# Kernel optimization log

Hardware: AMD Instinct MI355X
Metric: run time of the kernel (lower is better)

Reference implementation:

```python
import jax, jax.numpy as jnp
import numpy as np


def setup_inputs() -> dict:
    key = jax.random.key(0)
    x = jax.random.normal(key, (8, 128, 64, 64), dtype=jnp.float32)
    return {"x": x}


def reference(x) -> jnp.ndarray:
    # x: [B, d, c, c]; original uses a raw view (row-major reshape), not a permute.
    B, d, c, _ = x.shape
    n = c * c
    fch = x.reshape(B, n, d)                      # [B, N, d] reinterpretation of memory
    # self-similarity attention (no scaling): softmax(fch @ fch^T)
    attn = jax.nn.softmax(jnp.einsum('bnd,bmd->bnm', fch, fch), axis=-1)  # [B, N, N]
    out = jnp.einsum('bnd,bnm->bdm', fch, attn)   # fch^T @ attn -> [B, d, N]
    return out.reshape(B, d, c, c)
```

## Files before the change

### kernel.cpp

```cpp
#include <hip/hip_runtime.h>


typedef __attribute__((ext_vector_type(8))) __bf16 bf16x8;
typedef __attribute__((ext_vector_type(4))) float f32x4;
typedef __attribute__((ext_vector_type(4))) unsigned int u32x4;

#define MFMA16(a, b, c) __builtin_amdgcn_mfma_f32_16x16x32_bf16((a), (b), (c), 0, 0, 0)
#define GLOAD16(g, l)                                                       \
  __builtin_amdgcn_global_load_lds(                                         \
      (const __attribute__((address_space(1))) void*)(g),                   \
      (__attribute__((address_space(3))) void*)(l), 16, 0, 0)
#define GLOAD4(g, l)                                                        \
  __builtin_amdgcn_global_load_lds(                                         \
      (const __attribute__((address_space(1))) void*)(g),                   \
      (__attribute__((address_space(3))) void*)(l), 4, 0, 0)

static constexpr int NT = 4096;
static constexpr int DD = 128;
static constexpr float L2E = 1.4426950408889634f;

__device__ __forceinline__ unsigned short bfc(float f) {
  return __builtin_bit_cast(unsigned short, (__bf16)f);
}
__device__ __forceinline__ float bf2f(unsigned short u) {
  return (float)__builtin_bit_cast(__bf16, u);
}

__global__ __launch_bounds__(256) void cab_prep(const float* __restrict__ x,
                                                ushort* __restrict__ Fbb,
                                                ushort* __restrict__ FtF,
                                                float* __restrict__ nrm,
                                                float* __restrict__ bmax) {
  const int blk = blockIdx.x;
  const int b = blk & 7, n0 = (blk >> 3) * 64;
  const float* F = x + ((size_t)b * NT + n0) * DD;
  ushort* Fo = Fbb + ((size_t)b * NT + n0) * DD;
  ushort* To = FtF + (size_t)b * DD * NT;

  __shared__ ushort T[128 * 68];
  __shared__ float redw[4];

  const int t = threadIdx.x, seg = t & 15, rl = t >> 4;
  float lmax = 0.f;

#pragma unroll
  for (int i = 0; i < 4; ++i) {
    const int r = i * 16 + rl;
    float4 u = *(const float4*)(F + (size_t)r * DD + seg * 8);
    float4 v = *(const float4*)(F + (size_t)r * DD + seg * 8 + 4);
    ushort w[8] = {bfc(u.x), bfc(u.y), bfc(u.z), bfc(u.w),
                   bfc(v.x), bfc(v.y), bfc(v.z), bfc(v.w)};
    *(ushort4*)(Fo + (size_t)r * DD + seg * 8) = make_ushort4(w[0], w[1], w[2], w[3]);
    *(ushort4*)(Fo + (size_t)r * DD + seg * 8 + 4) = make_ushort4(w[4], w[5], w[6], w[7]);
    float s = 0.f;
#pragma unroll
    for (int j = 0; j < 8; ++j) {
      T[(seg * 8 + j) * 68 + r] = w[j];
      float f = bf2f(w[j]);
      s = fmaf(f, f, s);
    }
#pragma unroll
    for (int off = 1; off < 16; off <<= 1) s += __shfl_xor(s, off, 64);
    float rn = sqrtf(s);
    if (seg == 0) nrm[(size_t)b * NT + n0 + r] = rn;
    lmax = fmaxf(lmax, rn);
  }
#pragma unroll
  for (int off = 1; off < 64; off <<= 1) lmax = fmaxf(lmax, __shfl_xor(lmax, off, 64));
  if ((t & 63) == 0) redw[t >> 6] = lmax;
  __syncthreads();
  if (t == 0) bmax[blk] = fmaxf(fmaxf(redw[0], redw[1]), fmaxf(redw[2], redw[3]));

#pragma unroll
  for (int i = 0; i < 4; ++i) {
    int idx = i * 256 + t;
    int nh = idx >> 9, dt = (idx >> 6) & 7, ln = idx & 63;
    int d = dt * 16 + (ln & 15), nl = nh * 32 + (ln >> 4) * 8;
    const ushort* p = &T[d * 68 + nl];
    uint2 q0 = *(const uint2*)p;
    uint2 q1 = *(const uint2*)(p + 4);
    u32x4 q = {q0.x, q0.y, q1.x, q1.y};
    *(u32x4*)(To + (size_t)(((n0 >> 6) * 2 + nh) * 8 + dt) * 512 + ln * 8) = q;
  }
}

__global__ __launch_bounds__(64) void cab_mx(const float* __restrict__ bmax,
                                             float* __restrict__ mxf) {
  const int b = blockIdx.x, l = threadIdx.x;
  float m = bmax[l * 8 + b];
#pragma unroll
  for (int off = 1; off < 64; off <<= 1) m = fmaxf(m, __shfl_xor(m, off, 64));
  if (l == 0) mxf[b] = m;
}

__global__ __launch_bounds__(256, 4) void cab_rowstats(const ushort* __restrict__ Fbb,
                                                       const float* __restrict__ nrm,
                                                       const float* __restrict__ mxf,
                                                       float* __restrict__ c2g) {
  const int b = blockIdx.x & 7;
  const int nb = (blockIdx.x >> 3) * 64;
  const ushort* Fb = Fbb + (size_t)b * NT * DD;

  const int t = threadIdx.x, lane = t & 63, wv = t >> 6;
  const int lcol = lane & 15, hi = lane >> 4;
  const int nh = wv >> 1, mq = wv & 1;

  __shared__ __align__(16) char FmB[2][16384];
  __shared__ float zred[64];

  int fmoff[4];
#pragma unroll
  for (int i = 0; i < 4; ++i) {
    int L = i * 256 + t;
    int m = L >> 4, c = (L & 15) ^ (m & 15);
    fmoff[i] = m * DD + c * 8;
  }

  bf16x8 afr[2][4];
#pragma unroll
  for (int nt = 0; nt < 2; ++nt)
#pragma unroll
    for (int ks = 0; ks < 4; ++ks)
      afr[nt][ks] = *(const bf16x8*)(Fb + (size_t)(nb + nh * 32 + nt * 16 + lcol) * DD +
                                     ks * 32 + hi * 8);

  const float mxv = mxf[b] * L2E;
  float nsh[8];
#pragma unroll
  for (int nt = 0; nt < 2; ++nt)
#pragma unroll
    for (int r = 0; r < 4; ++r)
      nsh[nt * 4 + r] = -nrm[(size_t)b * NT + nb + nh * 32 + nt * 16 + hi * 4 + r] * mxv;

#pragma unroll
  for (int i = 0; i < 4; ++i) GLOAD16(Fb + fmoff[i], &FmB[0][i * 4096 + wv * 1024]);
  __syncthreads();

  float zloc[8];
#pragma unroll
  for (int i = 0; i < 8; ++i) zloc[i] = 0.f;

  for (int s = 0; s < 64; ++s) {
    const int cur = s & 1;
    if (s < 63) {
      const ushort* src = Fb + (size_t)(s + 1) * 64 * DD;
#pragma unroll
      for (int i = 0; i < 4; ++i)
        GLOAD16(src + fmoff[i], &FmB[cur ^ 1][i * 4096 + wv * 1024]);
    }

    f32x4 sacc[2][2];
#pragma unroll
    for (int nt = 0; nt < 2; ++nt)
#pragma unroll
      for (int ms = 0; ms < 2; ++ms) sacc[nt][ms] = (f32x4){0.f, 0.f, 0.f, 0.f};
#pragma unroll
    for (int ms = 0; ms < 2; ++ms)
#pragma unroll
      for (int ks = 0; ks < 4; ++ks) {
        int ml = mq * 32 + ms * 16 + lcol;
        bf16x8 bb = *(const bf16x8*)&FmB[cur][ml * 256 + (((ks * 4 + hi) ^ lcol) << 4)];
#pragma unroll
        for (int nt = 0; nt < 2; ++nt) sacc[nt][ms] = MFMA16(afr[nt][ks], bb, sacc[nt][ms]);
      }
#pragma unroll
    for (int nt = 0; nt < 2; ++nt)
#pragma unroll
      for (int r = 0; r < 4; ++r)
        zloc[nt * 4 + r] += __builtin_amdgcn_exp2f(fmaf(sacc[nt][0][r], L2E, nsh[nt * 4 + r])) +
                            __builtin_amdgcn_exp2f(fmaf(sacc[nt][1][r], L2E, nsh[nt * 4 + r]));
    __syncthreads();
  }

#pragma unroll
  for (int i = 0; i < 8; ++i) {
#pragma unroll
    for (int off = 1; off < 16; off <<= 1) zloc[i] += __shfl_xor(zloc[i], off, 64);
  }
  if (mq == 1 && lcol == 0) {
#pragma unroll
    for (int i = 0; i < 8; ++i) zred[nh * 32 + (i >> 2) * 16 + hi * 4 + (i & 3)] = zloc[i];
  }
  __syncthreads();
  if (mq == 0 && lcol == 0) {
#pragma unroll
    for (int i = 0; i < 8; ++i) {
      int nloc = nh * 32 + (i >> 2) * 16 + hi * 4 + (i & 3);
      c2g[(size_t)b * NT + nb + nloc] = nsh[i] - __log2f(zloc[i] + zred[nloc]);
    }
  }
}

__global__ __launch_bounds__(256, 2) void cab_out(const ushort* __restrict__ Fbb,
                                                  const ushort* __restrict__ FtF,
                                                  const float* __restrict__ c2g,
                                                  float* __restrict__ out) {
  const int b = blockIdx.x & 7, mb0 = (blockIdx.x >> 3) * 64;
  const ushort* Fb = Fbb + (size_t)b * NT * DD;
  const ushort* Fr = FtF + (size_t)b * DD * NT;
  const float* c2p = c2g + (size_t)b * NT;

  const int t = threadIdx.x, lane = t & 63, wv = t >> 6;
  const int lcol = lane & 15, hi = lane >> 4;
  const int mh = wv & 1, nh = wv >> 1;

  __shared__ __align__(16) char LB[42496];
  char* FnB = LB;
  char* Wt = LB + 32768;
  float* c2l = (float*)(LB + 41984);

  int fnoff[4];
#pragma unroll
  for (int i = 0; i < 4; ++i) {
    int L = i * 256 + t;
    int n = L >> 4, cn = (L & 15) ^ (n & 15);
    fnoff[i] = n * DD + cn * 8;
  }

  bf16x8 fmf[2][4];
#pragma unroll
  for (int ms = 0; ms < 2; ++ms)
#pragma unroll
    for (int ks = 0; ks < 4; ++ks)
      fmf[ms][ks] = *(const bf16x8*)(Fb + (size_t)(mb0 + mh * 32 + ms * 16 + lcol) * DD +
                                     ks * 32 + hi * 8);

  f32x4 accO[8][2];
#pragma unroll
  for (int dt = 0; dt < 8; ++dt)
#pragma unroll
    for (int ms = 0; ms < 2; ++ms) accO[dt][ms] = (f32x4){0.f, 0.f, 0.f, 0.f};

#pragma unroll
  for (int i = 0; i < 4; ++i) GLOAD16(Fb + fnoff[i], &FnB[i * 4096 + wv * 1024]);
  if (wv == 0) GLOAD4(c2p + lane, &c2l[0]);
  __syncthreads();

  const unsigned wtbase = wv * 2304;
  const ushort* a2w = Fr + (size_t)(nh * 8) * 512 + lane * 8;

  for (int s = 0; s < 64; ++s) {
    const int cur = s & 1;

    const ushort* ap = a2w + (size_t)s * 8192;
    bf16x8 a2[8];
#pragma unroll
    for (int dt = 0; dt < 8; ++dt) a2[dt] = *(const bf16x8*)(ap + dt * 512);

    if (s < 63) {
      const ushort* fs = Fb + (size_t)(s + 1) * 64 * DD;
#pragma unroll
      for (int i = 0; i < 4; ++i)
        GLOAD16(fs + fnoff[i], &FnB[(cur ^ 1) * 16384 + i * 4096 + wv * 1024]);
      if (wv == 0) GLOAD4(c2p + (s + 1) * 64 + lane, &c2l[((s + 1) & 1) * 64]);
    }

    f32x4 sacc[2][2];
#pragma unroll
    for (int nt = 0; nt < 2; ++nt)
#pragma unroll
      for (int ms = 0; ms < 2; ++ms) sacc[nt][ms] = (f32x4){0.f, 0.f, 0.f, 0.f};
#pragma unroll
    for (int nt = 0; nt < 2; ++nt)
#pragma unroll
      for (int ks = 0; ks < 4; ++ks) {
        int n = (nh * 2 + nt) * 16 + lcol;
        bf16x8 a = *(const bf16x8*)&FnB[cur * 16384 + n * 256 +
                                        (((ks * 4 + hi) ^ lcol) << 4)];
#pragma unroll
        for (int ms = 0; ms < 2; ++ms) sacc[nt][ms] = MFMA16(a, fmf[ms][ks], sacc[nt][ms]);
      }

#pragma unroll
    for (int nt = 0; nt < 2; ++nt) {
      float4 cv = *(const float4*)&c2l[(s & 1) * 64 + nh * 32 + nt * 16 + hi * 4];
#pragma unroll
      for (int ms = 0; ms < 2; ++ms) {
        ushort4 wp;
        wp.x = bfc(__builtin_amdgcn_exp2f(fmaf(sacc[nt][ms][0], L2E, cv.x)));
        wp.y = bfc(__builtin_amdgcn_exp2f(fmaf(sacc[nt][ms][1], L2E, cv.y)));
        wp.z = bfc(__builtin_amdgcn_exp2f(fmaf(sacc[nt][ms][2], L2E, cv.z)));
        wp.w = bfc(__builtin_amdgcn_exp2f(fmaf(sacc[nt][ms][3], L2E, cv.w)));
        *(ushort4*)&Wt[wtbase + (ms * 16 + lcol) * 72 + nt * 32 + hi * 8] = wp;
      }
    }

    bf16x8 b2[2];
#pragma unroll
    for (int ms = 0; ms < 2; ++ms) {
      const char* p = &Wt[wtbase + (ms * 16 + lcol) * 72 + hi * 16];
      uint2 lo = *(const uint2*)p;
      uint2 h2 = *(const uint2*)(p + 8);
      b2[ms] = __builtin_bit_cast(bf16x8, (u32x4){lo.x, lo.y, h2.x, h2.y});
    }
#pragma unroll
    for (int dt = 0; dt < 8; ++dt)
#pragma unroll
      for (int ms = 0; ms < 2; ++ms) accO[dt][ms] = MFMA16(a2[dt], b2[ms], accO[dt][ms]);

    __syncthreads();
  }

  float* red = (float*)LB;
  if (nh == 1) {
#pragma unroll
    for (int dt = 0; dt < 8; ++dt)
#pragma unroll
      for (int ms = 0; ms < 2; ++ms)
#pragma unroll
        for (int r = 0; r < 4; ++r)
          red[mh * 4096 + (dt * 8 + ms * 4 + r) * 64 + lane] = accO[dt][ms][r];
  }
  __syncthreads();
  if (nh == 0) {
    float* Ob = out + (size_t)b * DD * NT;
#pragma unroll
    for (int dt = 0; dt < 8; ++dt)
#pragma unroll
      for (int ms = 0; ms < 2; ++ms)
#pragma unroll
        for (int r = 0; r < 4; ++r) {
          float v = accO[dt][ms][r] + red[mh * 4096 + (dt * 8 + ms * 4 + r) * 64 + lane];
          Ob[(size_t)(dt * 16 + hi * 4 + r) * NT + mb0 + mh * 32 + ms * 16 + lcol] = v;
        }
  }
}

extern "C" void kernel_launch(void* const* d_in, const int* in_sizes, int n_in,
                              void* d_out, int out_size, void* d_ws, size_t ws_size,
                              hipStream_t stream) {
  const float* x = (const float*)d_in[0];
  float* out = (float*)d_out;
  char* ws = (char*)d_ws;
  ushort* Fbb = (ushort*)ws;
  ushort* FtF = (ushort*)(ws + (8u << 20));
  float* nrm = (float*)(ws + (16u << 20));
  float* bmax = (float*)(ws + (16u << 20) + 131072);
  float* mxf = (float*)(ws + (16u << 20) + 133120);
  float* c2 = (float*)(ws + (16u << 20) + 134144);

  hipLaunchKernelGGL(cab_prep, dim3(512), dim3(256), 0, stream, x, Fbb, FtF, nrm, bmax);
  hipLaunchKernelGGL(cab_mx, dim3(8), dim3(64), 0, stream, bmax, mxf);
  hipLaunchKernelGGL(cab_rowstats, dim3(512), dim3(256), 0, stream, Fbb, nrm, mxf, c2);
  hipLaunchKernelGGL(cab_out, dim3(512), dim3(256), 0, stream, Fbb, FtF, c2, out);
}
```

Measured before the change: 132.0 us.

## Load score-GEMM operand rows directly from global into registers, drop LDS staging

The cab_out kernel previously staged each 64-row block of F and the c2 log-normaliser values into double-buffered LDS with async global_load_lds, followed by a block-wide barrier per iteration. Each wave now loads its own bf16x8 fragments of F and the c2 float4 values straight from global memory into registers, and the per-iteration __syncthreads is removed. LDS use shrinks to the per-wave W tile, which may allow more resident blocks. The cost is more global/L2 traffic, since the two mh waves now each fetch the same rows, plus exposed load latency without explicit prefetch. The Wt region is per-wave, so dropping the barrier looks safe.

```diff
diff --git a/kernel.cpp b/kernel.cpp
--- a/kernel.cpp
+++ b/kernel.cpp
@@ -10,10 +10,6 @@
   __builtin_amdgcn_global_load_lds(                                         \
       (const __attribute__((address_space(1))) void*)(g),                   \
       (__attribute__((address_space(3))) void*)(l), 16, 0, 0)
-#define GLOAD4(g, l)                                                        \
-  __builtin_amdgcn_global_load_lds(                                         \
-      (const __attribute__((address_space(1))) void*)(g),                   \
-      (__attribute__((address_space(3))) void*)(l), 4, 0, 0)
 
 static constexpr int NT = 4096;
 static constexpr int DD = 128;
@@ -204,18 +200,8 @@
   const int lcol = lane & 15, hi = lane >> 4;
   const int mh = wv & 1, nh = wv >> 1;
 
-  __shared__ __align__(16) char LB[42496];
-  char* FnB = LB;
-  char* Wt = LB + 32768;
-  float* c2l = (float*)(LB + 41984);
-
-  int fnoff[4];
-#pragma unroll
-  for (int i = 0; i < 4; ++i) {
-    int L = i * 256 + t;
-    int n = L >> 4, cn = (L & 15) ^ (n & 15);
-    fnoff[i] = n * DD + cn * 8;
-  }
+  __shared__ __align__(16) char LB[32768];
+  char* Wt = LB;
 
   bf16x8 fmf[2][4];
 #pragma unroll
@@ -231,29 +217,28 @@
 #pragma unroll
     for (int ms = 0; ms < 2; ++ms) accO[dt][ms] = (f32x4){0.f, 0.f, 0.f, 0.f};
 
-#pragma unroll
-  for (int i = 0; i < 4; ++i) GLOAD16(Fb + fnoff[i], &FnB[i * 4096 + wv * 1024]);
-  if (wv == 0) GLOAD4(c2p + lane, &c2l[0]);
-  __syncthreads();
-
   const unsigned wtbase = wv * 2304;
   const ushort* a2w = Fr + (size_t)(nh * 8) * 512 + lane * 8;
+  const ushort* a1w = Fb + (size_t)(nh * 32 + lcol) * DD + hi * 8;
+  const float* cw = c2p + nh * 32 + hi * 4;
 
   for (int s = 0; s < 64; ++s) {
-    const int cur = s & 1;
-
     const ushort* ap = a2w + (size_t)s * 8192;
     bf16x8 a2[8];
 #pragma unroll
     for (int dt = 0; dt < 8; ++dt) a2[dt] = *(const bf16x8*)(ap + dt * 512);
 
-    if (s < 63) {
-      const ushort* fs = Fb + (size_t)(s + 1) * 64 * DD;
-#pragma unroll
-      for (int i = 0; i < 4; ++i)
-        GLOAD16(fs + fnoff[i], &FnB[(cur ^ 1) * 16384 + i * 4096 + wv * 1024]);
-      if (wv == 0) GLOAD4(c2p + (s + 1) * 64 + lane, &c2l[((s + 1) & 1) * 64]);
-    }
+    const ushort* rp = a1w + (size_t)s * 64 * DD;
+    bf16x8 a1[2][4];
+#pragma unroll
+    for (int nt = 0; nt < 2; ++nt)
+#pragma unroll
+      for (int ks = 0; ks < 4; ++ks)
+        a1[nt][ks] = *(const bf16x8*)(rp + nt * 16 * DD + ks * 32);
+
+    float4 cv[2];
+    cv[0] = *(const float4*)(cw + s * 64);
+    cv[1] = *(const float4*)(cw + s * 64 + 16);
 
     f32x4 sacc[2][2];
 #pragma unroll
@@ -263,24 +248,20 @@
 #pragma unroll
     for (int nt = 0; nt < 2; ++nt)
 #pragma unroll
-      for (int ks = 0; ks < 4; ++ks) {
-        int n = (nh * 2 + nt) * 16 + lcol;
-        bf16x8 a = *(const bf16x8*)&FnB[cur * 16384 + n * 256 +
-                                        (((ks * 4 + hi) ^ lcol) << 4)];
-#pragma unroll
-        for (int ms = 0; ms < 2; ++ms) sacc[nt][ms] = MFMA16(a, fmf[ms][ks], sacc[nt][ms]);
-      }
+      for (int ks = 0; ks < 4; ++ks)
+#pragma unroll
+        for (int ms = 0; ms < 2; ++ms)
+          sacc[nt][ms] = MFMA16(a1[nt][ks], fmf[ms][ks], sacc[nt][ms]);
 
 #pragma unroll
     for (int nt = 0; nt < 2; ++nt) {
-      float4 cv = *(const float4*)&c2l[(s & 1) * 64 + nh * 32 + nt * 16 + hi * 4];
 #pragma unroll
       for (int ms = 0; ms < 2; ++ms) {
         ushort4 wp;
-        wp.x = bfc(__builtin_amdgcn_exp2f(fmaf(sacc[nt][ms][0], L2E, cv.x)));
-        wp.y = bfc(__builtin_amdgcn_exp2f(fmaf(sacc[nt][ms][1], L2E, cv.y)));
-        wp.z = bfc(__builtin_amdgcn_exp2f(fmaf(sacc[nt][ms][2], L2E, cv.z)));
-        wp.w = bfc(__builtin_amdgcn_exp2f(fmaf(sacc[nt][ms][3], L2E, cv.w)));
+        wp.x = bfc(__builtin_amdgcn_exp2f(fmaf(sacc[nt][ms][0], L2E, cv[nt].x)));
+        wp.y = bfc(__builtin_amdgcn_exp2f(fmaf(sacc[nt][ms][1], L2E, cv[nt].y)));
+        wp.z = bfc(__builtin_amdgcn_exp2f(fmaf(sacc[nt][ms][2], L2E, cv[nt].z)));
+        wp.w = bfc(__builtin_amdgcn_exp2f(fmaf(sacc[nt][ms][3], L2E, cv[nt].w)));
         *(ushort4*)&Wt[wtbase + (ms * 16 + lcol) * 72 + nt * 32 + hi * 8] = wp;
       }
     }
@@ -297,10 +278,9 @@
     for (int dt = 0; dt < 8; ++dt)
 #pragma unroll
       for (int ms = 0; ms < 2; ++ms) accO[dt][ms] = MFMA16(a2[dt], b2[ms], accO[dt][ms]);
-
-    __syncthreads();
-  }
-
+  }
+
+  __syncthreads();
   float* red = (float*)LB;
   if (nh == 1) {
 #pragma unroll
```

Result: slower. 211.1 us (+59.9%).

## Triple-buffer output kernel LDS loads and fold block max into atomics

Applied to the files above, without the earlier changes.

The output kernel moves from double to triple buffering of the F tiles in shared memory. It prefetches two stages ahead with explicit vmcnt waits and sched barriers, and reads the c2 row statistics straight from global memory into registers instead of staging them through LDS. The separate max-reduction kernel is removed: each prep block does an atomicMax on the float bits into a memset-cleared buffer, which saves one launch. The cost is more LDS per block, which may limit occupancy. The hand-tuned waitcnt placement also carries some risk of ordering mistakes.

```diff
diff --git a/kernel.cpp b/kernel.cpp
--- a/kernel.cpp
+++ b/kernel.cpp
@@ -10,10 +10,12 @@
   __builtin_amdgcn_global_load_lds(                                         \
       (const __attribute__((address_space(1))) void*)(g),                   \
       (__attribute__((address_space(3))) void*)(l), 16, 0, 0)
-#define GLOAD4(g, l)                                                        \
-  __builtin_amdgcn_global_load_lds(                                         \
-      (const __attribute__((address_space(1))) void*)(g),                   \
-      (__attribute__((address_space(3))) void*)(l), 4, 0, 0)
+#define SBAR()                                                              \
+  do {                                                                      \
+    __builtin_amdgcn_sched_barrier(0);                                      \
+    __builtin_amdgcn_s_barrier();                                           \
+    __builtin_amdgcn_sched_barrier(0);                                      \
+  } while (0)
 
 static constexpr int NT = 4096;
 static constexpr int DD = 128;
@@ -30,7 +32,7 @@
                                                 ushort* __restrict__ Fbb,
                                                 ushort* __restrict__ FtF,
                                                 float* __restrict__ nrm,
-                                                float* __restrict__ bmax) {
+                                                unsigned int* __restrict__ mxfU) {
   const int blk = blockIdx.x;
   const int b = blk & 7, n0 = (blk >> 3) * 64;
   const float* F = x + ((size_t)b * NT + n0) * DD;
@@ -69,7 +71,10 @@
   for (int off = 1; off < 64; off <<= 1) lmax = fmaxf(lmax, __shfl_xor(lmax, off, 64));
   if ((t & 63) == 0) redw[t >> 6] = lmax;
   __syncthreads();
-  if (t == 0) bmax[blk] = fmaxf(fmaxf(redw[0], redw[1]), fmaxf(redw[2], redw[3]));
+  if (t == 0) {
+    float v = fmaxf(fmaxf(redw[0], redw[1]), fmaxf(redw[2], redw[3]));
+    atomicMax(mxfU + b, __float_as_uint(v));
+  }
 
 #pragma unroll
   for (int i = 0; i < 4; ++i) {
@@ -84,15 +89,6 @@
   }
 }
 
-__global__ __launch_bounds__(64) void cab_mx(const float* __restrict__ bmax,
-                                             float* __restrict__ mxf) {
-  const int b = blockIdx.x, l = threadIdx.x;
-  float m = bmax[l * 8 + b];
-#pragma unroll
-  for (int off = 1; off < 64; off <<= 1) m = fmaxf(m, __shfl_xor(m, off, 64));
-  if (l == 0) mxf[b] = m;
-}
-
 __global__ __launch_bounds__(256, 4) void cab_rowstats(const ushort* __restrict__ Fbb,
                                                        const float* __restrict__ nrm,
                                                        const float* __restrict__ mxf,
@@ -204,10 +200,8 @@
   const int lcol = lane & 15, hi = lane >> 4;
   const int mh = wv & 1, nh = wv >> 1;
 
-  __shared__ __align__(16) char LB[42496];
-  char* FnB = LB;
-  char* Wt = LB + 32768;
-  float* c2l = (float*)(LB + 41984);
+  __shared__ __align__(16) char LB[58368];
+  char* Wt = LB + 49152 + wv * 2304;
 
   int fnoff[4];
 #pragma unroll
@@ -231,30 +225,38 @@
 #pragma unroll
     for (int ms = 0; ms < 2; ++ms) accO[dt][ms] = (f32x4){0.f, 0.f, 0.f, 0.f};
 
-#pragma unroll
-  for (int i = 0; i < 4; ++i) GLOAD16(Fb + fnoff[i], &FnB[i * 4096 + wv * 1024]);
-  if (wv == 0) GLOAD4(c2p + lane, &c2l[0]);
-  __syncthreads();
-
-  const unsigned wtbase = wv * 2304;
   const ushort* a2w = Fr + (size_t)(nh * 8) * 512 + lane * 8;
-
+  const float* cw = c2p + nh * 32 + hi * 4;
+
+#pragma unroll
+  for (int i = 0; i < 4; ++i) GLOAD16(Fb + fnoff[i], &LB[i * 4096 + wv * 1024]);
+#pragma unroll
+  for (int i = 0; i < 4; ++i)
+    GLOAD16(Fb + 64 * DD + fnoff[i], &LB[16384 + i * 4096 + wv * 1024]);
+  __builtin_amdgcn_sched_barrier(0);
+  asm volatile("s_waitcnt vmcnt(4)" ::: "memory");
+  SBAR();
+
+  int rb = 0, db = 2;
   for (int s = 0; s < 64; ++s) {
-    const int cur = s & 1;
-
+    __builtin_amdgcn_sched_barrier(0);
+    bf16x8 a2[8];
     const ushort* ap = a2w + (size_t)s * 8192;
-    bf16x8 a2[8];
 #pragma unroll
     for (int dt = 0; dt < 8; ++dt) a2[dt] = *(const bf16x8*)(ap + dt * 512);
-
-    if (s < 63) {
-      const ushort* fs = Fb + (size_t)(s + 1) * 64 * DD;
-#pragma unroll
-      for (int i = 0; i < 4; ++i)
-        GLOAD16(fs + fnoff[i], &FnB[(cur ^ 1) * 16384 + i * 4096 + wv * 1024]);
-      if (wv == 0) GLOAD4(c2p + (s + 1) * 64 + lane, &c2l[((s + 1) & 1) * 64]);
-    }
-
+    float4 cv0 = *(const float4*)(cw + s * 64);
+    float4 cv1 = *(const float4*)(cw + s * 64 + 16);
+    __builtin_amdgcn_sched_barrier(0);
+
+    if (s < 62) {
+      const ushort* fs = Fb + (size_t)(s + 2) * 64 * DD;
+      char* dst = LB + db * 16384;
+#pragma unroll
+      for (int i = 0; i < 4; ++i) GLOAD16(fs + fnoff[i], dst + i * 4096 + wv * 1024);
+    }
+    __builtin_amdgcn_sched_barrier(0);
+
+    const char* FnB = LB + rb * 16384;
     f32x4 sacc[2][2];
 #pragma unroll
     for (int nt = 0; nt < 2; ++nt)
@@ -265,15 +267,14 @@
 #pragma unroll
       for (int ks = 0; ks < 4; ++ks) {
         int n = (nh * 2 + nt) * 16 + lcol;
-        bf16x8 a = *(const bf16x8*)&FnB[cur * 16384 + n * 256 +
-                                        (((ks * 4 + hi) ^ lcol) << 4)];
+        bf16x8 a = *(const bf16x8*)&FnB[n * 256 + (((ks * 4 + hi) ^ lcol) << 4)];
 #pragma unroll
         for (int ms = 0; ms < 2; ++ms) sacc[nt][ms] = MFMA16(a, fmf[ms][ks], sacc[nt][ms]);
       }
 
 #pragma unroll
     for (int nt = 0; nt < 2; ++nt) {
-      float4 cv = *(const float4*)&c2l[(s & 1) * 64 + nh * 32 + nt * 16 + hi * 4];
+      float4 cv = nt ? cv1 : cv0;
 #pragma unroll
       for (int ms = 0; ms < 2; ++ms) {
         ushort4 wp;
@@ -281,14 +282,14 @@
         wp.y = bfc(__builtin_amdgcn_exp2f(fmaf(sacc[nt][ms][1], L2E, cv.y)));
         wp.z = bfc(__builtin_amdgcn_exp2f(fmaf(sacc[nt][ms][2], L2E, cv.z)));
         wp.w = bfc(__builtin_amdgcn_exp2f(fmaf(sacc[nt][ms][3], L2E, cv.w)));
-        *(ushort4*)&Wt[wtbase + (ms * 16 + lcol) * 72 + nt * 32 + hi * 8] = wp;
+        *(ushort4*)&Wt[(ms * 16 + lcol) * 72 + nt * 32 + hi * 8] = wp;
       }
     }
 
     bf16x8 b2[2];
 #pragma unroll
     for (int ms = 0; ms < 2; ++ms) {
-      const char* p = &Wt[wtbase + (ms * 16 + lcol) * 72 + hi * 16];
+      const char* p = &Wt[(ms * 16 + lcol) * 72 + hi * 16];
       uint2 lo = *(const uint2*)p;
       uint2 h2 = *(const uint2*)(p + 8);
       b2[ms] = __builtin_bit_cast(bf16x8, (u32x4){lo.x, lo.y, h2.x, h2.y});
@@ -298,9 +299,12 @@
 #pragma unroll
       for (int ms = 0; ms < 2; ++ms) accO[dt][ms] = MFMA16(a2[dt], b2[ms], accO[dt][ms]);
 
-    __syncthreads();
-  }
-
+    SBAR();
+    rb = (rb == 2) ? 0 : rb + 1;
+    db = (db == 2) ? 0 : db + 1;
+  }
+
+  __syncthreads();
   float* red = (float*)LB;
   if (nh == 1) {
 #pragma unroll
@@ -335,12 +339,12 @@
   ushort* Fbb = (ushort*)ws;
   ushort* FtF = (ushort*)(ws + (8u << 20));
   float* nrm = (float*)(ws + (16u << 20));
-  float* bmax = (float*)(ws + (16u << 20) + 131072);
-  float* mxf = (float*)(ws + (16u << 20) + 133120);
-  float* c2 = (float*)(ws + (16u << 20) + 134144);
-
-  hipLaunchKernelGGL(cab_prep, dim3(512), dim3(256), 0, stream, x, Fbb, FtF, nrm, bmax);
-  hipLaunchKernelGGL(cab_mx, dim3(8), dim3(64), 0, stream, bmax, mxf);
+  float* mxf = (float*)(ws + (16u << 20) + 131072);
+  float* c2 = (float*)(ws + (16u << 20) + 132096);
+
+  hipMemsetAsync(mxf, 0, 8 * sizeof(float), stream);
+  hipLaunchKernelGGL(cab_prep, dim3(512), dim3(256), 0, stream, x, Fbb, FtF, nrm,
+                     (unsigned int*)mxf);
   hipLaunchKernelGGL(cab_rowstats, dim3(512), dim3(256), 0, stream, Fbb, nrm, mxf, c2);
   hipLaunchKernelGGL(cab_out, dim3(512), dim3(256), 0, stream, Fbb, FtF, c2, out);
 }
```

Result: slower. 146.6 us (+11.0%).
